# Performance work log

Hardware: AMD Instinct MI355X
Metric: run time of the kernel (lower is better)

Reference implementation:

```python
import math
import jax, jax.numpy as jnp
from jax import lax
import numpy as np

PATCHES = [(8, 8), (4, 4), (2, 2), (1, 1)]  # (width, height) per scale
BN_EPS = 1e-5


def setup_inputs() -> dict:
    key = jax.random.key(0)
    ks = jax.random.split(key, 9)
    b, d, h, w = 4, 256, 64, 64
    s = 1.0 / math.sqrt(d)
    return {
        "x": jax.random.normal(ks[0], (b, d, h, w), jnp.float32),
        "wq": jax.random.normal(ks[1], (d, d), jnp.float32) * s,
        "bq": jax.random.normal(ks[2], (d,), jnp.float32) * 0.02,
        "wk": jax.random.normal(ks[3], (d, d), jnp.float32) * s,
        "bk": jax.random.normal(ks[4], (d,), jnp.float32) * 0.02,
        "wv": jax.random.normal(ks[5], (d, d), jnp.float32) * s,
        "bv": jax.random.normal(ks[6], (d,), jnp.float32) * 0.02,
        "w_out": jax.random.normal(ks[7], (d, d, 3, 3), jnp.float32) * (s / 3.0),
        "b_out": jax.random.normal(ks[8], (d,), jnp.float32) * 0.02,
        "gamma": jnp.ones((d,), jnp.float32),
        "beta": jnp.zeros((d,), jnp.float32),
    }


def _to_tokens(t, b, dk, out_h, ph, out_w, pw):
    # [b, dk, h, w] -> [b, out_h*out_w, dk*ph*pw]
    t = t.reshape(b, dk, out_h, ph, out_w, pw)
    t = t.transpose(0, 2, 4, 1, 3, 5)
    return t.reshape(b, out_h * out_w, dk * ph * pw)


def reference(x, wq, bq, wk, bk, wv, bv, w_out, b_out, gamma, beta):
    b, c, h, w = x.shape
    # 1x1 conv projections == channel matmuls
    q = jnp.einsum('bchw,oc->bohw', x, wq) + bq[None, :, None, None]
    k = jnp.einsum('bchw,oc->bohw', x, wk) + bk[None, :, None, None]
    v = jnp.einsum('bchw,oc->bohw', x, wv) + bv[None, :, None, None]

    dk = c // len(PATCHES)
    outs = []
    for i, (pw, ph) in enumerate(PATCHES):
        sl = slice(i * dk, (i + 1) * dk)
        out_h, out_w = h // ph, w // pw
        Q = _to_tokens(q[:, sl], b, dk, out_h, ph, out_w, pw)
        K = _to_tokens(k[:, sl], b, dk, out_h, ph, out_w, pw)
        V = _to_tokens(v[:, sl], b, dk, out_h, ph, out_w, pw)
        scores = jnp.einsum('bnd,bmd->bnm', Q, K) / math.sqrt(Q.shape[-1])
        p = jax.nn.softmax(scores, axis=-1)
        y = jnp.einsum('bnm,bmd->bnd', p, V)
        # tokens -> [b, dk, h, w]
        y = y.reshape(b, out_h, out_w, dk, ph, pw)
        y = y.transpose(0, 3, 1, 4, 2, 5).reshape(b, dk, h, w)
        outs.append(y)
    out = jnp.concatenate(outs, axis=1)

    # 3x3 conv, padding=1
    z = lax.conv_general_dilated(out, w_out, (1, 1), 'SAME',
                                 dimension_numbers=('NCHW', 'OIHW', 'NCHW'))
    z = z + b_out[None, :, None, None]
    # BatchNorm2d (training-mode batch stats)
    mean = jnp.mean(z, axis=(0, 2, 3), keepdims=True)
    var = jnp.var(z, axis=(0, 2, 3), keepdims=True)
    zn = (z - mean) * lax.rsqrt(var + BN_EPS)
    zn = zn * gamma[None, :, None, None] + beta[None, :, None, None]
    # LeakyReLU(0.2)
    return jnp.where(zn > 0, zn, 0.2 * zn)
```

## Files before the change

### kernel.cpp

```cpp
#include <hip/hip_runtime.h>
#include <cmath>


#define OFF_XB  0LL
#define OFF_QB  2097152LL
#define OFF_SS  8388608LL
#define OFF_PP  12582912LL
#define OFF_YT  14680064LL
#define OFF_WQK 18874368LL
#define OFF_BIA 18972672LL
#define OFF_WCV 18973440LL
#define OFF_STT 19268352LL
#define OFF_SP0 19268864LL
#define OFF_S1  19399936LL
#define OFF_P0  19662080LL
#define OFF_P1  19670272LL

#define FC 0.18033688f
#define CSHIFT 6.0f

typedef __attribute__((ext_vector_type(8))) short short8;
typedef __attribute__((ext_vector_type(4))) float f32x4;

__device__ inline unsigned short f2bf(float f) {
  unsigned u = __float_as_uint(f);
  u += 0x7fff + ((u >> 16) & 1);
  return (unsigned short)(u >> 16);
}

__device__ inline unsigned cvt_pk_bf16(float a, float b) {
  unsigned r;
  asm("v_cvt_pk_bf16_f32 %0, %1, %2" : "=v"(r) : "v"(a), "v"(b));
  return r;
}

__global__ __launch_bounds__(256) void prep_k(
    const float* __restrict__ x, unsigned short* __restrict__ xb,
    const float* __restrict__ wq, const float* __restrict__ wk,
    const float* __restrict__ wv, const float* __restrict__ bq,
    const float* __restrict__ bk, const float* __restrict__ bv,
    unsigned short* __restrict__ Wqkv, float* __restrict__ biasQKV,
    const float* __restrict__ wcv, unsigned short* __restrict__ Wcb)
{
  const int bid = blockIdx.x, t = threadIdx.x;
  if (bid < 256) {
    __shared__ unsigned short rowb[256][66];
    const int b = bid >> 6, y = bid & 63;
    for (int i = t; i < 16384; i += 256) {
      int c = i >> 6, xx = i & 63;
      rowb[c][xx] = f2bf(x[((long long)(b*256 + c) << 12) + (y << 6) + xx]);
    }
    __syncthreads();
    unsigned int* outw = (unsigned int*)(xb + ((long long)bid << 14));
    for (int i = t; i < 8192; i += 256) {
      int xx = i >> 7, c2 = (i & 127) * 2;
      outw[xx*128 + (c2 >> 1)] = (unsigned)rowb[c2][xx]
                               | ((unsigned)rowb[c2+1][xx] << 16);
    }
  } else if (bid < 1024) {
    const int row = bid - 256;
    const int which = row >> 8, oc = row & 255;
    const float* src = which == 0 ? wq : which == 1 ? wk : wv;
    Wqkv[row*256 + t] = f2bf(src[oc*256 + t]);
    if (row < 3) {
      const float* bs = row == 0 ? bq : row == 1 ? bk : bv;
      biasQKV[row*256 + t] = bs[t];
    }
  } else {
    int i = (bid - 1024)*256 + t;
    int tap = i >> 16, oc = (i >> 8) & 255, ic = i & 255;
    Wcb[i] = f2bf(wcv[((long long)(oc*256 + ic))*9 + tap]);
  }
}

template<int EPI>
__device__ void gemm_nt_body(
    const unsigned short* __restrict__ A, const unsigned short* __restrict__ B,
    void* __restrict__ Cv, const float* __restrict__ bias,
    int M, int N, int K, int lda, int ldb, int ldc,
    long long sA, long long sB, long long sC, float alpha,
    int bx, int by, int bz)
{
  const int t = threadIdx.x, l = t & 63;
  const int lr = l & 15, lg = l >> 4;
  const int w = t >> 6, wm = w >> 1, wn = w & 1;
  const int m0 = by*128 + wm*64, n0 = bx*128 + wn*64;
  if (m0 >= M || n0 >= N) return;
  const unsigned short* Ab = A + (long long)bz*sA + (long long)(m0 + lr)*lda + lg*8;
  const unsigned short* Bb = B + (long long)bz*sB + (long long)(n0 + lr)*ldb + lg*8;

  f32x4 acc[4][4] = {};
#pragma unroll 2
  for (int kk = 0; kk < K; kk += 32) {
    short8 af[4], bf[4];
#pragma unroll
    for (int i = 0; i < 4; i++)
      af[i] = *(const short8*)(Ab + (long long)i*16*lda + kk);
#pragma unroll
    for (int i = 0; i < 4; i++)
      bf[i] = *(const short8*)(Bb + (long long)i*16*ldb + kk);
#pragma unroll
    for (int mf = 0; mf < 4; mf++)
#pragma unroll
      for (int nf = 0; nf < 4; nf++)
        acc[mf][nf] = __builtin_amdgcn_mfma_f32_16x16x32_bf16(
            af[mf], bf[nf], acc[mf][nf], 0, 0, 0);
  }

  if (EPI == 0) {
    float* C = (float*)Cv + (long long)bz*sC;
#pragma unroll
    for (int mf = 0; mf < 4; mf++)
#pragma unroll
      for (int r = 0; r < 4; r++) {
        const int row = m0 + mf*16 + lg*4 + r;
#pragma unroll
        for (int nf = 0; nf < 4; nf++)
          C[(long long)row*ldc + n0 + nf*16 + lr] = acc[mf][nf][r] * alpha;
      }
  } else {
    unsigned short* Qbase = (unsigned short*)Cv;
#pragma unroll
    for (int mf = 0; mf < 4; mf++)
#pragma unroll
      for (int r = 0; r < 4; r++) {
        const int gi = m0 + mf*16 + lg*4 + r;
        const int which = gi >> 8, ch = gi & 255;
        const int scale = ch >> 6, c = ch & 63;
        const int sh = 3 - scale, msk = (1 << sh) - 1;
        const bool tr = (which == 2);
        const float bb = bias[gi];
        unsigned short* dst = Qbase + (long long)which*4194304
                            + (long long)scale*1048576 + (long long)bz*262144;
#pragma unroll
        for (int nf = 0; nf < 4; nf++) {
          const int gj = n0 + nf*16 + lr;
          const int y = gj >> 6, xx = gj & 63;
          const int n = (y >> sh)*(64 >> sh) + (xx >> sh);
          const int d = (c << (2*sh)) + ((y & msk) << sh) + (xx & msk);
          const long long idx = tr
              ? (long long)d*(4096 >> (2*sh)) + n
              : (long long)n*(64 << (2*sh)) + d;
          dst[idx] = f2bf(acc[mf][nf][r] + bb);
        }
      }
  }
}

__global__ __launch_bounds__(256) void qkv_k(
    const unsigned short* __restrict__ Wqkv, const unsigned short* __restrict__ xb,
    unsigned short* __restrict__ Qu, const float* __restrict__ biasQKV)
{
  gemm_nt_body<1>(Wqkv, xb, (void*)Qu, biasQKV, 768, 4096, 256, 256, 256, 0,
                  0, 1048576, 0, 1.0f, blockIdx.x, blockIdx.y, blockIdx.z);
}

__device__ void s0_scores_wave(
    const unsigned short* __restrict__ Q, const unsigned short* __restrict__ K,
    float* __restrict__ Sp, int bid)
{
  const int t = threadIdx.x, l = t & 63, w = t >> 6;
  const int lr = l & 15, lg = l >> 4;
  const int task = bid*4 + w;
  const int b = task >> 3, ks = task & 7;
  const unsigned short* Qb = Q + (long long)b*262144;
  const unsigned short* Kb = K + (long long)b*262144;
  f32x4 acc[4][4] = {};
  const int k0 = ks*512;
#pragma unroll 2
  for (int kk = k0; kk < k0 + 512; kk += 32) {
    short8 af[4], bf[4];
#pragma unroll
    for (int i = 0; i < 4; i++)
      af[i] = *(const short8*)(Qb + (long long)(i*16 + lr)*4096 + kk + lg*8);
#pragma unroll
    for (int i = 0; i < 4; i++)
      bf[i] = *(const short8*)(Kb + (long long)(i*16 + lr)*4096 + kk + lg*8);
#pragma unroll
    for (int mf = 0; mf < 4; mf++)
#pragma unroll
      for (int nf = 0; nf < 4; nf++)
        acc[mf][nf] = __builtin_amdgcn_mfma_f32_16x16x32_bf16(
            af[mf], bf[nf], acc[mf][nf], 0, 0, 0);
  }
#pragma unroll
  for (int mf = 0; mf < 4; mf++)
#pragma unroll
    for (int r = 0; r < 4; r++) {
      const int row = mf*16 + lg*4 + r;
#pragma unroll
      for (int nf = 0; nf < 4; nf++)
        Sp[(((long long)(ks*4 + b)*64 + row) << 6) + nf*16 + lr]
            = acc[mf][nf][r];
    }
}

__device__ void flash3_body(
    const unsigned short* __restrict__ Q3, const unsigned short* __restrict__ K3,
    const unsigned short* __restrict__ Vt3, unsigned short* __restrict__ inb,
    int bx, int b)
{
  constexpr int LD = 72;
  __shared__ unsigned short KVs[2][2][64*LD];
  __shared__ unsigned short Ps[64*LD];
  const int t = threadIdx.x, l = t & 63, w = t >> 6;
  const int lr = l & 15, lg = l >> 4;
  const int q0 = bx * 64;
  const long long base = (long long)b * 262144;
  const unsigned short* Qg = Q3 + base;
  const unsigned short* Kg = K3 + base;
  const unsigned short* Vg = Vt3 + base;

  short8 bq[2];
  bq[0] = *(const short8*)(Qg + (long long)(q0 + w*16 + lr)*64 + lg*8);
  bq[1] = *(const short8*)(Qg + (long long)(q0 + w*16 + lr)*64 + 32 + lg*8);

  f32x4 acc[4] = {};
  float li = 0.f;

  const int r_ = t >> 3, c8_ = (t & 7) * 8;
  uint4 kreg[2], vreg[2];

#define LOADKV(KT) do { \
    const int k0_ = (KT) * 64; \
    _Pragma("unroll") \
    for (int it = 0; it < 2; it++) { \
      const int rr = r_ + it*32; \
      kreg[it] = *(const uint4*)(Kg + (long long)(k0_ + rr)*64 + c8_); \
      vreg[it] = *(const uint4*)(Vg + (long long)rr*4096 + k0_ + c8_); \
    } } while (0)
#define STOREKV(BUF) do { \
    _Pragma("unroll") \
    for (int it = 0; it < 2; it++) { \
      const int rr = r_ + it*32; \
      *(uint4*)(KVs[BUF][0] + rr*LD + c8_) = kreg[it]; \
      *(uint4*)(KVs[BUF][1] + rr*LD + c8_) = vreg[it]; \
    } } while (0)

  LOADKV(0);
  STOREKV(0);
  __syncthreads();

  for (int kt = 0; kt < 64; ++kt) {
    if (kt < 63) LOADKV(kt + 1);
    const unsigned short* Ksb = KVs[kt & 1][0];
    const unsigned short* Vsb = KVs[kt & 1][1];
    f32x4 s[4];
#pragma unroll
    for (int cf = 0; cf < 4; cf++) {
      short8 ak0 = *(const short8*)(Ksb + (cf*16 + lr)*LD + lg*8);
      short8 ak1 = *(const short8*)(Ksb + (cf*16 + lr)*LD + 32 + lg*8);
      f32x4 zz = {};
      zz = __builtin_amdgcn_mfma_f32_16x16x32_bf16(ak0, bq[0], zz, 0,0,0);
      s[cf] = __builtin_amdgcn_mfma_f32_16x16x32_bf16(ak1, bq[1], zz, 0,0,0);
    }
    float p[16], psum = 0.f;
#pragma unroll
    for (int cf = 0; cf < 4; cf++)
#pragma unroll
      for (int r = 0; r < 4; r++) {
        float e = exp2f(fmaf(s[cf][r], FC, -CSHIFT));
        p[cf*4 + r] = e; psum += e;
      }
    li += psum;
    {
      unsigned short* pr = Ps + (w*16 + lr)*LD;
#pragma unroll
      for (int cf = 0; cf < 4; cf++) {
        *(unsigned*)(pr + cf*16 + lg*4)     = cvt_pk_bf16(p[cf*4+0], p[cf*4+1]);
        *(unsigned*)(pr + cf*16 + lg*4 + 2) = cvt_pk_bf16(p[cf*4+2], p[cf*4+3]);
      }
    }
    short8 bp0 = *(const short8*)(Ps + (w*16 + lr)*LD + lg*8);
    short8 bp1 = *(const short8*)(Ps + (w*16 + lr)*LD + 32 + lg*8);
#pragma unroll
    for (int df = 0; df < 4; df++) {
      short8 av0 = *(const short8*)(Vsb + (df*16 + lr)*LD + lg*8);
      short8 av1 = *(const short8*)(Vsb + (df*16 + lr)*LD + 32 + lg*8);
      acc[df] = __builtin_amdgcn_mfma_f32_16x16x32_bf16(av0, bp0, acc[df], 0,0,0);
      acc[df] = __builtin_amdgcn_mfma_f32_16x16x32_bf16(av1, bp1, acc[df], 0,0,0);
    }
    if (kt < 63) {
      STOREKV((kt + 1) & 1);
      __syncthreads();
    }
  }
#undef LOADKV
#undef STOREKV
  li += __shfl_xor(li, 16);
  li += __shfl_xor(li, 32);
  const float inv = 1.f / li;
  const long long row = (long long)b*4096 + q0 + w*16 + lr;
  unsigned short* ob = inb + row*256 + 192 + lg*4;
#pragma unroll
  for (int df = 0; df < 4; df++) {
    unsigned w0 = cvt_pk_bf16(acc[df][0]*inv, acc[df][1]*inv);
    unsigned w1 = cvt_pk_bf16(acc[df][2]*inv, acc[df][3]*inv);
    *(unsigned*)(ob + df*16)     = w0;
    *(unsigned*)(ob + df*16 + 2) = w1;
  }
}

__global__ __launch_bounds__(256) void stageA_k(
    const unsigned short* __restrict__ Qu, const unsigned short* __restrict__ Ku,
    const unsigned short* __restrict__ Vu,
    float* __restrict__ Sp0, float* __restrict__ S1, float* __restrict__ S2,
    unsigned short* __restrict__ inb)
{
  const int bid = blockIdx.x;
  if (bid < 256) {
    flash3_body(Qu+3145728, Ku+3145728, Vu+3145728, inb, bid & 63, bid >> 6);
  } else if (bid < 264) {
    s0_scores_wave(Qu, Ku, Sp0, bid - 256);
  } else if (bid < 280) {
    int q = bid - 264;
    gemm_nt_body<0>(Qu+1048576, Ku+1048576, (void*)S1, nullptr,
        256, 256, 1024, 1024, 1024, 256, 262144, 262144, 65536, 0.03125f,
        q & 1, (q >> 1) & 1, q >> 2);
  } else {
    int q = bid - 280;
    gemm_nt_body<0>(Qu+2097152, Ku+2097152, (void*)S2, nullptr,
        1024, 1024, 256, 256, 256, 1024, 262144, 262144, 1048576, 0.0625f,
        q & 7, (q >> 3) & 7, q >> 6);
  }
}

template<int CNT>
__device__ void softmax_row(const float* __restrict__ S,
                            unsigned short* __restrict__ P, long long row)
{
  const int l = threadIdx.x & 63;
  const float* p = S + row*(CNT*64);
  unsigned short* o = P + row*(CNT*64);
  float v[CNT];
  float mx = -1e30f;
#pragma unroll
  for (int i = 0; i < CNT; i++) { v[i] = p[i*64 + l]; mx = fmaxf(mx, v[i]); }
#pragma unroll
  for (int off = 1; off < 64; off <<= 1) mx = fmaxf(mx, __shfl_xor(mx, off, 64));
  float sum = 0.f;
#pragma unroll
  for (int i = 0; i < CNT; i++) { v[i] = __expf(v[i] - mx); sum += v[i]; }
#pragma unroll
  for (int off = 1; off < 64; off <<= 1) sum += __shfl_xor(sum, off, 64);
  const float inv = 1.f / sum;
#pragma unroll
  for (int i = 0; i < CNT; i++) o[i*64 + l] = f2bf(v[i] * inv);
}

__global__ __launch_bounds__(256) void stageB_k(
    const float* __restrict__ Sp0, unsigned short* __restrict__ P0,
    const float* __restrict__ S1, unsigned short* __restrict__ P1,
    const float* __restrict__ S2, unsigned short* __restrict__ P2)
{
  const int bid = blockIdx.x, t = threadIdx.x, l = t & 63, w = t >> 6;
  if (bid < 1024) {
    softmax_row<16>(S2, P2, (long long)bid*4 + w);
  } else if (bid < 1280) {
    softmax_row<4>(S1, P1, (long long)(bid - 1024)*4 + w);
  } else {
    const int row = (bid - 1280)*4 + w;
    const int b = row >> 6, r = row & 63;
    float v = 0.f;
#pragma unroll
    for (int ks = 0; ks < 8; ks++)
      v += Sp0[(((long long)(ks*4 + b)*64 + r) << 6) + l];
    v *= 0.015625f;
    float mx = v;
#pragma unroll
    for (int off = 1; off < 64; off <<= 1) mx = fmaxf(mx, __shfl_xor(mx, off, 64));
    float e = __expf(v - mx), sum = e;
#pragma unroll
    for (int off = 1; off < 64; off <<= 1) sum += __shfl_xor(sum, off, 64);
    P0[(row << 6) + l] = f2bf(e / sum);
  }
}

__global__ __launch_bounds__(256) void stageC_k(
    const unsigned short* __restrict__ P0, const unsigned short* __restrict__ P1,
    const unsigned short* __restrict__ P2, const unsigned short* __restrict__ Vu,
    float* __restrict__ Yt)
{
  const int bid = blockIdx.x;
  if (bid < 128) {
    int q = bid;
    gemm_nt_body<0>(P0, Vu, (void*)Yt, nullptr,
        64, 4096, 64, 64, 64, 4096, 4096, 262144, 262144, 1.0f,
        q & 31, 0, q >> 5);
  } else if (bid < 192) {
    int q = bid - 128;
    gemm_nt_body<0>(P1, Vu+1048576, (void*)(Yt+1048576), nullptr,
        256, 1024, 256, 256, 256, 1024, 65536, 262144, 262144, 1.0f,
        q & 7, (q >> 3) & 1, q >> 4);
  } else {
    int q = bid - 192;
    gemm_nt_body<0>(P2, Vu+2097152, (void*)(Yt+2097152), nullptr,
        1024, 256, 1024, 1024, 1024, 256, 1048576, 262144, 262144, 1.0f,
        q & 1, (q >> 1) & 7, q >> 4);
  }
}

__global__ __launch_bounds__(256) void unpack_nhwc_k(
    const float* __restrict__ Yt, unsigned short* __restrict__ inb)
{
  __shared__ unsigned short rowb[192][66];
  const int b = blockIdx.x >> 6, y = blockIdx.x & 63;
  const int t = threadIdx.x;
  for (int i = t; i < 12288; i += 256) {
    int ch = i >> 6, x = i & 63;
    int scale = ch >> 6, c = ch & 63;
    int sh = 3 - scale, msk = (1 << sh) - 1;
    int n = (y >> sh) * (64 >> sh) + (x >> sh);
    int d = (c << (2*sh)) + ((y & msk) << sh) + (x & msk);
    rowb[ch][x] = f2bf(Yt[(long long)scale*1048576 + ((long long)b << 18)
                          + (long long)n * (64 << (2*sh)) + d]);
  }
  __syncthreads();
  unsigned int* outw = (unsigned int*)(inb + ((long long)blockIdx.x << 14));
  for (int i = t; i < 6144; i += 256) {
    int xx = i / 96, cw = i % 96;
    outw[xx*128 + cw] = (unsigned)rowb[cw*2][xx]
                      | ((unsigned)rowb[cw*2+1][xx] << 16);
  }
}

__global__ __launch_bounds__(512) void conv_mfma_k(
    const unsigned short* __restrict__ inb, const unsigned short* __restrict__ Wb,
    const float* __restrict__ bias, float* __restrict__ z)
{
  __shared__ unsigned short lds[2][6*66*32];
  const int t = threadIdx.x;
  const int l = t & 63, wid = t >> 6;
  const int lr = l & 15, lg = l >> 4;
  const int waveM = wid >> 2, waveN = wid & 3;
  const int b = blockIdx.x >> 4, y0 = (blockIdx.x & 15) * 4;
  const int oc0 = blockIdx.y * 64 + waveM * 32;
  const long long inbase = (long long)b * 1048576;
  const int kgrp = lg * 8;

  f32x4 acc[2][4] = {};
  uint4 sreg[4];

#define CLOAD(IC0) do { \
    _Pragma("unroll") \
    for (int i = 0; i < 4; i++) { \
      int q = t + i*512; \
      if (q < 1584) { \
        int ic8 = q & 3, cc = (q >> 2) % 66, rr = q / 264; \
        int gy = y0 - 1 + rr, gx = cc - 1; \
        uint4 v = make_uint4(0u,0u,0u,0u); \
        if ((unsigned)gy < 64u && (unsigned)gx < 64u) \
          v = *(const uint4*)(inb + inbase + ((long long)(gy*64+gx))*256 \
                              + (IC0) + ic8*8); \
        sreg[i] = v; \
      } \
    } } while (0)
#define CSTORE(BUF) do { \
    _Pragma("unroll") \
    for (int i = 0; i < 4; i++) { \
      int q = t + i*512; \
      if (q < 1584) *(uint4*)(&lds[BUF][q*8]) = sreg[i]; \
    } } while (0)

  CLOAD(0);
  CSTORE(0);
  __syncthreads();

  for (int c = 0; c < 8; ++c) {
    const int ic0 = c * 32;
    if (c < 7) CLOAD(ic0 + 32);
    const unsigned short* wbase = Wb + (long long)(oc0 + lr)*256 + ic0 + kgrp;
    short8 afr[9][2];
#pragma unroll
    for (int tap = 0; tap < 9; tap++) {
      afr[tap][0] = *(const short8*)(wbase + (long long)tap*65536);
      afr[tap][1] = *(const short8*)(wbase + (long long)tap*65536 + 16*256);
    }
    const unsigned short* L = lds[c & 1];
#pragma unroll
    for (int ky = 0; ky < 3; ky++) {
#pragma unroll
      for (int kx = 0; kx < 3; kx++) {
        const int tap = ky*3 + kx;
#pragma unroll
        for (int nf = 0; nf < 4; nf++) {
          int pix = waveN*64 + nf*16 + lr;
          int rp = pix >> 6, xx = pix & 63;
          short8 bf = *(const short8*)(L + ((rp + ky)*66 + xx + kx)*32 + kgrp);
          acc[0][nf] = __builtin_amdgcn_mfma_f32_16x16x32_bf16(
              afr[tap][0], bf, acc[0][nf], 0, 0, 0);
          acc[1][nf] = __builtin_amdgcn_mfma_f32_16x16x32_bf16(
              afr[tap][1], bf, acc[1][nf], 0, 0, 0);
        }
      }
    }
    if (c < 7) {
      CSTORE((c + 1) & 1);
      __syncthreads();
    }
  }
#undef CLOAD
#undef CSTORE

  const long long zb = ((long long)b * 256) << 12;
#pragma unroll
  for (int mf = 0; mf < 2; mf++) {
#pragma unroll
    for (int r = 0; r < 4; r++) {
      const int oc = oc0 + mf*16 + lg*4 + r;
      const float bb = bias[oc];
      const long long rowbase = zb + ((long long)oc << 12) + y0*64;
#pragma unroll
      for (int nf = 0; nf < 4; nf++) {
        int pix = waveN*64 + nf*16 + lr;
        z[rowbase + pix] = acc[mf][nf][r] + bb;
      }
    }
  }
}

__global__ __launch_bounds__(256) void bn_stats_k(
    const float* __restrict__ z, float* __restrict__ stats)
{
  const int ch = blockIdx.x, t = threadIdx.x;
  float s = 0.f, q = 0.f;
  for (int b = 0; b < 4; b++) {
    const float* p = z + ((long long)(b*256 + ch) << 12);
    for (int i = t; i < 4096; i += 256) { float v = p[i]; s += v; q += v*v; }
  }
  __shared__ float rs[256], rq[256];
  rs[t] = s; rq[t] = q; __syncthreads();
  for (int st = 128; st > 0; st >>= 1) {
    if (t < st) { rs[t] += rs[t+st]; rq[t] += rq[t+st]; }
    __syncthreads();
  }
  if (t == 0) {
    float mean = rs[0] * (1.f/16384.f);
    float var  = rq[0] * (1.f/16384.f) - mean*mean;
    stats[ch]       = mean;
    stats[256 + ch] = rsqrtf(var + 1e-5f);
  }
}

__global__ __launch_bounds__(256) void bn_apply_k(
    const float* __restrict__ z, const float* __restrict__ stats,
    const float* __restrict__ gamma, const float* __restrict__ beta,
    float* __restrict__ out)
{
  long long i4 = ((long long)blockIdx.x*256 + threadIdx.x) * 4;
  int ch = (int)((i4 >> 12) & 255);
  float mean = stats[ch], rsg = stats[256 + ch];
  float g = gamma[ch], bt = beta[ch];
  float4 v = *(const float4*)(z + i4);
  float r[4] = {v.x, v.y, v.z, v.w};
#pragma unroll
  for (int j = 0; j < 4; j++) {
    float u = (r[j] - mean) * rsg * g + bt;
    r[j] = u > 0.f ? u : 0.2f * u;
  }
  *(float4*)(out + i4) = make_float4(r[0], r[1], r[2], r[3]);
}

extern "C" void kernel_launch(void* const* d_in, const int* in_sizes, int n_in,
                              void* d_out, int out_size, void* d_ws, size_t ws_size,
                              hipStream_t stream)
{
  const float* x     = (const float*)d_in[0];
  const float* wq    = (const float*)d_in[1];
  const float* bq    = (const float*)d_in[2];
  const float* wk    = (const float*)d_in[3];
  const float* bk    = (const float*)d_in[4];
  const float* wv    = (const float*)d_in[5];
  const float* bv    = (const float*)d_in[6];
  const float* w_out = (const float*)d_in[7];
  const float* b_out = (const float*)d_in[8];
  const float* gamma = (const float*)d_in[9];
  const float* beta  = (const float*)d_in[10];
  float* out = (float*)d_out;

  float* ws = (float*)d_ws;
  unsigned short* xb  = (unsigned short*)(ws + OFF_XB);
  unsigned short* Qu  = (unsigned short*)(ws + OFF_QB);
  unsigned short* Ku  = Qu + 4194304;
  unsigned short* Vu  = Qu + 8388608;
  float* S2  = ws + OFF_SS;
  unsigned short* P2 = (unsigned short*)(ws + OFF_PP);
  float* Yt  = ws + OFF_YT;
  unsigned short* Wqk = (unsigned short*)(ws + OFF_WQK);
  float* biasQ = ws + OFF_BIA;
  unsigned short* Wcv = (unsigned short*)(ws + OFF_WCV);
  float* St  = ws + OFF_STT;
  float* Sp0 = ws + OFF_SP0;
  float* S1  = ws + OFF_S1;
  unsigned short* P0 = (unsigned short*)(ws + OFF_P0);
  unsigned short* P1 = (unsigned short*)(ws + OFF_P1);
  unsigned short* inb = (unsigned short*)(ws + OFF_XB);
  float* z = Yt;

  dim3 blk(256);

  prep_k<<<dim3(3328), blk, 0, stream>>>(
      x, xb, wq, wk, wv, bq, bk, bv, Wqk, biasQ, w_out, Wcv);

  qkv_k<<<dim3(32,6,4), blk, 0, stream>>>(Wqk, xb, Qu, biasQ);

  stageA_k<<<dim3(536), blk, 0, stream>>>(Qu, Ku, Vu, Sp0, S1, S2, inb);

  stageB_k<<<dim3(1344), blk, 0, stream>>>(Sp0, P0, S1, P1, S2, P2);

  stageC_k<<<dim3(256), blk, 0, stream>>>(P0, P1, P2, Vu, Yt);

  unpack_nhwc_k<<<dim3(256), blk, 0, stream>>>(Yt, inb);

  conv_mfma_k<<<dim3(64,4), dim3(512), 0, stream>>>(inb, Wcv, b_out, z);

  bn_stats_k<<<dim3(256), blk, 0, stream>>>(z, St);
  bn_apply_k<<<dim3(4096), blk, 0, stream>>>(z, St, gamma, beta, out);
}
```

Measured before the change: 244.2 us.

## Split scale-3 flash attention over keys and fuse unpack into PV epilogues

The scale-3 flash attention is split four ways over the key dimension, giving 1024 blocks instead of 256. Each block writes fp32 partial outputs and row sums, and stageB gains blocks that combine the partials and write bf16 NHWC input for the conv. The PV GEMMs for the other scales now write directly into the NHWC conv input through a new epilogue, which removes the separate unpack kernel and the fp32 Yt round trip. In exchange, the split adds traffic for the partials and relies on the fixed exp shift being safe to sum across splits without a max correction.

```diff
diff --git a/kernel.cpp b/kernel.cpp
--- a/kernel.cpp
+++ b/kernel.cpp
@@ -15,6 +15,7 @@
 #define OFF_S1  19399936LL
 #define OFF_P0  19662080LL
 #define OFF_P1  19670272LL
+#define OFF_LI  19801344LL
 
 #define FC 0.18033688f
 #define CSHIFT 6.0f
@@ -73,7 +74,7 @@
   }
 }
 
-template<int EPI>
+template<int EPI, int SH = 0>
 __device__ void gemm_nt_body(
     const unsigned short* __restrict__ A, const unsigned short* __restrict__ B,
     void* __restrict__ Cv, const float* __restrict__ bias,
@@ -118,7 +119,7 @@
         for (int nf = 0; nf < 4; nf++)
           C[(long long)row*ldc + n0 + nf*16 + lr] = acc[mf][nf][r] * alpha;
       }
-  } else {
+  } else if (EPI == 1) {
     unsigned short* Qbase = (unsigned short*)Cv;
 #pragma unroll
     for (int mf = 0; mf < 4; mf++)
@@ -142,6 +143,26 @@
               ? (long long)d*(4096 >> (2*sh)) + n
               : (long long)n*(64 << (2*sh)) + d;
           dst[idx] = f2bf(acc[mf][nf][r] + bb);
+        }
+      }
+  } else {
+    unsigned short* inb = (unsigned short*)Cv;
+    constexpr int msk = (1 << SH) - 1;
+    constexpr int scale = 3 - SH;
+#pragma unroll
+    for (int mf = 0; mf < 4; mf++)
+#pragma unroll
+      for (int r = 0; r < 4; r++) {
+        const int gi = m0 + mf*16 + lg*4 + r;
+        const int ty = gi >> (6 - SH), tx = gi & ((64 >> SH) - 1);
+#pragma unroll
+        for (int nf = 0; nf < 4; nf++) {
+          const int gj = n0 + nf*16 + lr;
+          const int c = gj >> (2*SH);
+          const int y = (ty << SH) | ((gj >> SH) & msk);
+          const int x = (tx << SH) | (gj & msk);
+          inb[((((long long)bz << 12) + (y << 6) + x) << 8) + scale*64 + c]
+              = f2bf(acc[mf][nf][r]);
         }
       }
   }
@@ -197,8 +218,8 @@
 
 __device__ void flash3_body(
     const unsigned short* __restrict__ Q3, const unsigned short* __restrict__ K3,
-    const unsigned short* __restrict__ Vt3, unsigned short* __restrict__ inb,
-    int bx, int b)
+    const unsigned short* __restrict__ Vt3, float* __restrict__ part,
+    float* __restrict__ lig, int bx, int b, int sp)
 {
   constexpr int LD = 72;
   __shared__ unsigned short KVs[2][2][64*LD];
@@ -237,14 +258,16 @@
       *(uint4*)(KVs[BUF][1] + rr*LD + c8_) = vreg[it]; \
     } } while (0)
 
-  LOADKV(0);
+  const int kt0 = sp * 16;
+  LOADKV(kt0);
   STOREKV(0);
   __syncthreads();
 
-  for (int kt = 0; kt < 64; ++kt) {
-    if (kt < 63) LOADKV(kt + 1);
-    const unsigned short* Ksb = KVs[kt & 1][0];
-    const unsigned short* Vsb = KVs[kt & 1][1];
+  for (int i = 0; i < 16; ++i) {
+    const int kt = kt0 + i;
+    if (i < 15) LOADKV(kt + 1);
+    const unsigned short* Ksb = KVs[i & 1][0];
+    const unsigned short* Vsb = KVs[i & 1][1];
     f32x4 s[4];
 #pragma unroll
     for (int cf = 0; cf < 4; cf++) {
@@ -280,8 +303,8 @@
       acc[df] = __builtin_amdgcn_mfma_f32_16x16x32_bf16(av0, bp0, acc[df], 0,0,0);
       acc[df] = __builtin_amdgcn_mfma_f32_16x16x32_bf16(av1, bp1, acc[df], 0,0,0);
     }
-    if (kt < 63) {
-      STOREKV((kt + 1) & 1);
+    if (i < 15) {
+      STOREKV((i + 1) & 1);
       __syncthreads();
     }
   }
@@ -289,36 +312,33 @@
 #undef STOREKV
   li += __shfl_xor(li, 16);
   li += __shfl_xor(li, 32);
-  const float inv = 1.f / li;
-  const long long row = (long long)b*4096 + q0 + w*16 + lr;
-  unsigned short* ob = inb + row*256 + 192 + lg*4;
-#pragma unroll
-  for (int df = 0; df < 4; df++) {
-    unsigned w0 = cvt_pk_bf16(acc[df][0]*inv, acc[df][1]*inv);
-    unsigned w1 = cvt_pk_bf16(acc[df][2]*inv, acc[df][3]*inv);
-    *(unsigned*)(ob + df*16)     = w0;
-    *(unsigned*)(ob + df*16 + 2) = w1;
-  }
+  const long long prow = (long long)(sp*4 + b)*4096 + q0 + w*16 + lr;
+#pragma unroll
+  for (int df = 0; df < 4; df++)
+    *(float4*)(part + prow*64 + df*16 + lg*4) =
+        make_float4(acc[df][0], acc[df][1], acc[df][2], acc[df][3]);
+  if (lg == 0) lig[prow] = li;
 }
 
 __global__ __launch_bounds__(256) void stageA_k(
     const unsigned short* __restrict__ Qu, const unsigned short* __restrict__ Ku,
     const unsigned short* __restrict__ Vu,
     float* __restrict__ Sp0, float* __restrict__ S1, float* __restrict__ S2,
-    unsigned short* __restrict__ inb)
+    float* __restrict__ part, float* __restrict__ lig)
 {
   const int bid = blockIdx.x;
-  if (bid < 256) {
-    flash3_body(Qu+3145728, Ku+3145728, Vu+3145728, inb, bid & 63, bid >> 6);
-  } else if (bid < 264) {
-    s0_scores_wave(Qu, Ku, Sp0, bid - 256);
-  } else if (bid < 280) {
-    int q = bid - 264;
+  if (bid < 1024) {
+    flash3_body(Qu+3145728, Ku+3145728, Vu+3145728, part, lig,
+                bid & 63, (bid >> 6) & 3, bid >> 8);
+  } else if (bid < 1032) {
+    s0_scores_wave(Qu, Ku, Sp0, bid - 1024);
+  } else if (bid < 1048) {
+    int q = bid - 1032;
     gemm_nt_body<0>(Qu+1048576, Ku+1048576, (void*)S1, nullptr,
         256, 256, 1024, 1024, 1024, 256, 262144, 262144, 65536, 0.03125f,
         q & 1, (q >> 1) & 1, q >> 2);
   } else {
-    int q = bid - 280;
+    int q = bid - 1048;
     gemm_nt_body<0>(Qu+2097152, Ku+2097152, (void*)S2, nullptr,
         1024, 1024, 256, 256, 256, 1024, 262144, 262144, 1048576, 0.0625f,
         q & 7, (q >> 3) & 7, q >> 6);
@@ -351,14 +371,16 @@
 __global__ __launch_bounds__(256) void stageB_k(
     const float* __restrict__ Sp0, unsigned short* __restrict__ P0,
     const float* __restrict__ S1, unsigned short* __restrict__ P1,
-    const float* __restrict__ S2, unsigned short* __restrict__ P2)
+    const float* __restrict__ S2, unsigned short* __restrict__ P2,
+    const float* __restrict__ part, const float* __restrict__ lig,
+    unsigned short* __restrict__ inb)
 {
   const int bid = blockIdx.x, t = threadIdx.x, l = t & 63, w = t >> 6;
   if (bid < 1024) {
     softmax_row<16>(S2, P2, (long long)bid*4 + w);
   } else if (bid < 1280) {
     softmax_row<4>(S1, P1, (long long)(bid - 1024)*4 + w);
-  } else {
+  } else if (bid < 1344) {
     const int row = (bid - 1280)*4 + w;
     const int b = row >> 6, r = row & 63;
     float v = 0.f;
@@ -373,54 +395,50 @@
 #pragma unroll
     for (int off = 1; off < 64; off <<= 1) sum += __shfl_xor(sum, off, 64);
     P0[(row << 6) + l] = f2bf(e / sum);
+  } else {
+    const long long row = (long long)(bid - 1344)*64 + (t >> 2);
+    const int dd = (t & 3) * 16;
+    float L = 0.f;
+#pragma unroll
+    for (int s = 0; s < 4; s++) L += lig[(long long)s*16384 + row];
+    const float inv = 1.f / L;
+#pragma unroll
+    for (int j = 0; j < 4; j++) {
+      float ax = 0.f, ay = 0.f, az = 0.f, aw = 0.f;
+#pragma unroll
+      for (int s = 0; s < 4; s++) {
+        float4 v = *(const float4*)(part + ((long long)s*16384 + row)*64 + dd + j*4);
+        ax += v.x; ay += v.y; az += v.z; aw += v.w;
+      }
+      ushort4 ov;
+      ov.x = f2bf(ax*inv); ov.y = f2bf(ay*inv);
+      ov.z = f2bf(az*inv); ov.w = f2bf(aw*inv);
+      *(ushort4*)(inb + row*256 + 192 + dd + j*4) = ov;
+    }
   }
 }
 
 __global__ __launch_bounds__(256) void stageC_k(
     const unsigned short* __restrict__ P0, const unsigned short* __restrict__ P1,
     const unsigned short* __restrict__ P2, const unsigned short* __restrict__ Vu,
-    float* __restrict__ Yt)
+    unsigned short* __restrict__ inb)
 {
   const int bid = blockIdx.x;
   if (bid < 128) {
     int q = bid;
-    gemm_nt_body<0>(P0, Vu, (void*)Yt, nullptr,
-        64, 4096, 64, 64, 64, 4096, 4096, 262144, 262144, 1.0f,
+    gemm_nt_body<2,3>(P0, Vu, (void*)inb, nullptr,
+        64, 4096, 64, 64, 64, 0, 4096, 262144, 0, 1.0f,
         q & 31, 0, q >> 5);
   } else if (bid < 192) {
     int q = bid - 128;
-    gemm_nt_body<0>(P1, Vu+1048576, (void*)(Yt+1048576), nullptr,
-        256, 1024, 256, 256, 256, 1024, 65536, 262144, 262144, 1.0f,
+    gemm_nt_body<2,2>(P1, Vu+1048576, (void*)inb, nullptr,
+        256, 1024, 256, 256, 256, 0, 65536, 262144, 0, 1.0f,
         q & 7, (q >> 3) & 1, q >> 4);
   } else {
     int q = bid - 192;
-    gemm_nt_body<0>(P2, Vu+2097152, (void*)(Yt+2097152), nullptr,
-        1024, 256, 1024, 1024, 1024, 256, 1048576, 262144, 262144, 1.0f,
+    gemm_nt_body<2,1>(P2, Vu+2097152, (void*)inb, nullptr,
+        1024, 256, 1024, 1024, 1024, 0, 1048576, 262144, 0, 1.0f,
         q & 1, (q >> 1) & 7, q >> 4);
-  }
-}
-
-__global__ __launch_bounds__(256) void unpack_nhwc_k(
-    const float* __restrict__ Yt, unsigned short* __restrict__ inb)
-{
-  __shared__ unsigned short rowb[192][66];
-  const int b = blockIdx.x >> 6, y = blockIdx.x & 63;
-  const int t = threadIdx.x;
-  for (int i = t; i < 12288; i += 256) {
-    int ch = i >> 6, x = i & 63;
-    int scale = ch >> 6, c = ch & 63;
-    int sh = 3 - scale, msk = (1 << sh) - 1;
-    int n = (y >> sh) * (64 >> sh) + (x >> sh);
-    int d = (c << (2*sh)) + ((y & msk) << sh) + (x & msk);
-    rowb[ch][x] = f2bf(Yt[(long long)scale*1048576 + ((long long)b << 18)
-                          + (long long)n * (64 << (2*sh)) + d]);
-  }
-  __syncthreads();
-  unsigned int* outw = (unsigned int*)(inb + ((long long)blockIdx.x << 14));
-  for (int i = t; i < 6144; i += 256) {
-    int xx = i / 96, cw = i % 96;
-    outw[xx*128 + cw] = (unsigned)rowb[cw*2][xx]
-                      | ((unsigned)rowb[cw*2+1][xx] << 16);
   }
 }
 
@@ -585,7 +603,7 @@
   unsigned short* Vu  = Qu + 8388608;
   float* S2  = ws + OFF_SS;
   unsigned short* P2 = (unsigned short*)(ws + OFF_PP);
-  float* Yt  = ws + OFF_YT;
+  float* part = ws + OFF_YT;
   unsigned short* Wqk = (unsigned short*)(ws + OFF_WQK);
   float* biasQ = ws + OFF_BIA;
   unsigned short* Wcv = (unsigned short*)(ws + OFF_WCV);
@@ -594,8 +612,9 @@
   float* S1  = ws + OFF_S1;
   unsigned short* P0 = (unsigned short*)(ws + OFF_P0);
   unsigned short* P1 = (unsigned short*)(ws + OFF_P1);
+  float* lig = ws + OFF_LI;
   unsigned short* inb = (unsigned short*)(ws + OFF_XB);
-  float* z = Yt;
+  float* z = ws + OFF_YT;
 
   dim3 blk(256);
 
@@ -604,13 +623,12 @@
 
   qkv_k<<<dim3(32,6,4), blk, 0, stream>>>(Wqk, xb, Qu, biasQ);
 
-  stageA_k<<<dim3(536), blk, 0, stream>>>(Qu, Ku, Vu, Sp0, S1, S2, inb);
-
-  stageB_k<<<dim3(1344), blk, 0, stream>>>(Sp0, P0, S1, P1, S2, P2);
-
-  stageC_k<<<dim3(256), blk, 0, stream>>>(P0, P1, P2, Vu, Yt);
-
-  unpack_nhwc_k<<<dim3(256), blk, 0, stream>>>(Yt, inb);
+  stageA_k<<<dim3(1304), blk, 0, stream>>>(Qu, Ku, Vu, Sp0, S1, S2, part, lig);
+
+  stageB_k<<<dim3(1600), blk, 0, stream>>>(
+      Sp0, P0, S1, P1, S2, P2, part, lig, inb);
+
+  stageC_k<<<dim3(256), blk, 0, stream>>>(P0, P1, P2, Vu, inb);
 
   conv_mfma_k<<<dim3(64,4), dim3(512), 0, stream>>>(inb, Wcv, b_out, z);
 
```

New measurement: 246.8 us. About the same (+1.1%).
